# Optimization experiments

Hardware: AMD Instinct MI355X
Metric: run time of the kernel (lower is better)

## Reference

```python
import jax, jax.numpy as jnp
import numpy as np
from jax import lax


def ternarize(w):
    """Standard TWN ternarization with straight-through estimator.
    delta = 0.7*mean(|w|); alpha = mean(|w|) over kept entries; w_t = alpha*sign(w)*mask.
    """
    a = jnp.abs(w)
    delta = 0.7 * a.mean()
    mask = (a > delta).astype(w.dtype)
    alpha = (a * mask).sum() / jnp.maximum(mask.sum(), 1.0)
    wt = alpha * jnp.sign(w) * mask
    return w + lax.stop_gradient(wt - w)  # STE


def conv3x3(x, w, b):
    y = lax.conv_general_dilated(x, ternarize(w), window_strides=(1, 1),
                                 padding=((1, 1), (1, 1)),
                                 dimension_numbers=('NCHW', 'OIHW', 'NCHW'))
    return y + b[None, :, None, None]


def maxpool2(x):
    return lax.reduce_window(x, -jnp.inf, lax.max, (1, 1, 2, 2), (1, 1, 2, 2), 'VALID')


def setup_inputs() -> dict:
    key = jax.random.key(0)
    ks = jax.random.split(key, 11)
    s = lambda k, shape, scale: jax.random.normal(k, shape, dtype=jnp.float32) * scale
    return {
        'x':   s(ks[0], (1024, 3, 32, 32), 1.0),
        'w1':  s(ks[1], (64, 3, 3, 3), 0.1),
        'b1':  s(ks[2], (64,), 0.01),
        'w2':  s(ks[3], (128, 64, 3, 3), 0.05),
        'b2':  s(ks[4], (128,), 0.01),
        'w3':  s(ks[5], (256, 128, 3, 3), 0.03),
        'b3':  s(ks[6], (256,), 0.01),
        'wf1': s(ks[7], (256, 4096), 0.02),
        'bf1': s(ks[8], (256,), 0.01),
        'wf2': s(ks[9], (10, 256), 0.06),
        'bf2': s(ks[10], (10,), 0.01),
    }


def reference(x, w1, b1, w2, b2, w3, b3, wf1, bf1, wf2, bf2):
    x = maxpool2(jax.nn.relu(conv3x3(x, w1, b1)))   # [B,64,16,16]
    x = maxpool2(jax.nn.relu(conv3x3(x, w2, b2)))   # [B,128,8,8]
    x = maxpool2(jax.nn.relu(conv3x3(x, w3, b3)))   # [B,256,4,4]
    x = x.reshape(-1, 256 * 4 * 4)
    x = jax.nn.relu(x @ ternarize(wf1).T + bf1)     # [B,256]
    return x @ ternarize(wf2).T + bf2               # [B,10]
```

## Files before the change

kernel.cpp:

```cpp
#include <hip/hip_runtime.h>
#include <hip/hip_bf16.h>


typedef __attribute__((ext_vector_type(8))) short short8;
typedef __attribute__((ext_vector_type(4))) float f32x4;
typedef __attribute__((ext_vector_type(4))) int i32x4;

#define GLOAD_LDS16(g, l)                                              \
    __builtin_amdgcn_global_load_lds(                                  \
        (const __attribute__((address_space(1))) void*)(g),            \
        (__attribute__((address_space(3))) void*)(l), 16, 0, 0)

__device__ __forceinline__ unsigned short f2bf(float x) {
    unsigned u = __float_as_uint(x);
    return (unsigned short)((u + 0x7fffu + ((u >> 16) & 1u)) >> 16);
}
__device__ __forceinline__ float bf2f(unsigned short b) {
    return __uint_as_float(((unsigned)b) << 16);
}

__device__ __forceinline__ float calc_S1(const double* __restrict__ scr,
                                         float amaxx) {
    const int* ii = (const int*)(scr + 20);
    const double c2 = scr[2];
    const float alpha1 = (float)(scr[1] / (c2 > 1.0 ? c2 : 1.0));
    const float ub = alpha1 * (float)ii[3] * amaxx + __int_as_float(ii[6]);
    return 32512.0f / fmaxf(ub, 1e-30f);
}
__device__ __forceinline__ float calc_S2(const double* __restrict__ scr,
                                         float amax1) {
    const int* ii = (const int*)(scr + 20);
    const double c2 = scr[6];
    const float alpha2 = (float)(scr[5] / (c2 > 1.0 ? c2 : 1.0));
    const float ub = alpha2 * (float)ii[4] * amax1 + __int_as_float(ii[7]);
    return 32512.0f / fmaxf(ub, 1e-30f);
}
__device__ __forceinline__ float calc_S3(const double* __restrict__ scr,
                                         float amax2) {
    const int* ii = (const int*)(scr + 20);
    const double c2 = scr[10];
    const float alpha3 = (float)(scr[9] / (c2 > 1.0 ? c2 : 1.0));
    const float ub = alpha3 * (float)ii[5] * amax2 + __int_as_float(ii[8]);
    return 32512.0f / fmaxf(ub, 1e-30f);
}

#define WS_W1B   0
#define N_W1B    2048
#define WS_W2P   (WS_W1B + N_W1B)
#define N_W2P    (9*128*64)
#define WS_W3P   (WS_W2P + N_W2P)
#define N_W3P    (9*256*128)
#define WS_WTF1  (WS_W3P + N_W3P)
#define N_WTF1   (256*4096)
#define WS_WTF2  (WS_WTF1 + N_WTF1)
#define N_WTF2   (10*256)
#define WS_A1    (WS_WTF2 + N_WTF2)
#define N_A1     (1024*256*64)
#define WS_A2    (WS_A1 + N_A1)
#define N_A2     (1024*64*128)
#define WS_A3    (WS_A2 + N_A2)
#define N_A3     (1024*16*256)
#define WS_F1    (WS_A3 + N_A3)
#define N_F1     (1024*256)
#define WS_SCR   (WS_F1 + N_F1)

#define FC1_S    8

struct TernArgs {
    const float* w[6];
    int n[6];
};

__global__ void tern_stats1(TernArgs ta, double* __restrict__ scr) {
    const int wi = blockIdx.y;
    const float* __restrict__ w = ta.w[wi];
    const int n = ta.n[wi];
    __shared__ double red[4];
    const int lane = threadIdx.x & 63, wv = threadIdx.x >> 6;
    if (wi == 5) {
        float m = 0.f;
        for (int i = blockIdx.x * blockDim.x + threadIdx.x; i < n;
             i += gridDim.x * blockDim.x)
            m = fmaxf(m, fabsf(w[i]));
        #pragma unroll
        for (int off = 32; off > 0; off >>= 1)
            m = fmaxf(m, __shfl_down(m, off, 64));
        if (lane == 0) red[wv] = (double)m;
        __syncthreads();
        if (threadIdx.x == 0) {
            float mm = (float)fmax(fmax(red[0], red[1]), fmax(red[2], red[3]));
            atomicMax((int*)(scr + 20), __float_as_int(mm));
        }
        return;
    }
    double s = 0.0;
    for (int i = blockIdx.x * blockDim.x + threadIdx.x; i < n;
         i += gridDim.x * blockDim.x)
        s += (double)fabsf(w[i]);
    #pragma unroll
    for (int off = 32; off > 0; off >>= 1) s += __shfl_down(s, off, 64);
    if (lane == 0) red[wv] = s;
    __syncthreads();
    if (threadIdx.x == 0)
        atomicAdd(scr + wi * 4, red[0] + red[1] + red[2] + red[3]);
}

__global__ void tern_stats2(TernArgs ta,
                            const float* __restrict__ b1v,
                            const float* __restrict__ b2v,
                            const float* __restrict__ b3v,
                            signed char* __restrict__ w1b,
                            signed char* __restrict__ w2p8,
                            signed char* __restrict__ w3p8,
                            signed char* __restrict__ wtf1b8,
                            signed char* __restrict__ wtf2b8,
                            double* __restrict__ scr) {
    const int wi = blockIdx.y;
    const int lane = threadIdx.x & 63, wv = threadIdx.x >> 6;

    if (wi == 5) {
        int* ii = (int*)(scr + 20);
        const int gw = blockIdx.x * 4 + wv;
        if (gw < 64) {
            const float d = (float)(0.7 * scr[0] / 1728.0);
            const float* row = ta.w[0] + gw * 27;
            int c = (lane < 27) ? (fabsf(row[lane]) > d ? 1 : 0) : 0;
            #pragma unroll
            for (int off = 32; off > 0; off >>= 1)
                c += __shfl_down(c, off, 64);
            if (lane == 0) atomicMax(ii + 3, c);
        } else if (gw < 192) {
            const float d = (float)(0.7 * scr[4] / 73728.0);
            const float* row = ta.w[1] + (long)(gw - 64) * 576;
            int c = 0;
            for (int k = lane; k < 576; k += 64)
                c += (fabsf(row[k]) > d) ? 1 : 0;
            #pragma unroll
            for (int off = 32; off > 0; off >>= 1)
                c += __shfl_down(c, off, 64);
            if (lane == 0) atomicMax(ii + 4, c);
        } else if (gw < 448) {
            const float d = (float)(0.7 * scr[8] / 294912.0);
            const float* row = ta.w[2] + (long)(gw - 192) * 1152;
            int c = 0;
            for (int k = lane; k < 1152; k += 64)
                c += (fabsf(row[k]) > d) ? 1 : 0;
            #pragma unroll
            for (int off = 32; off > 0; off >>= 1)
                c += __shfl_down(c, off, 64);
            if (lane == 0) atomicMax(ii + 5, c);
        } else if (gw < 451) {
            const float* bv = (gw == 448) ? b1v : (gw == 449) ? b2v : b3v;
            const int nb = (gw == 448) ? 64 : (gw == 449) ? 128 : 256;
            float m = 0.f;
            for (int k = lane; k < nb; k += 64) m = fmaxf(m, fabsf(bv[k]));
            #pragma unroll
            for (int off = 32; off > 0; off >>= 1)
                m = fmaxf(m, __shfl_down(m, off, 64));
            if (lane == 0)
                atomicMax(ii + 6 + (gw - 448), __float_as_int(m));
        }
        return;
    }

    const float* __restrict__ w = ta.w[wi];
    const int n = ta.n[wi];
    const float delta = (float)(0.7 * scr[wi * 4] / (double)n);

    if (wi == 0) {
        const int z0 = blockIdx.x * blockDim.x + threadIdx.x;
        const int zstride = gridDim.x * blockDim.x;
        for (int i = z0; i < 8192; i += zstride) {
            const int k = i & 63;
            const int plane = i >> 12;
            const bool sign_slot = plane == 0 ? (k < 27)
                                              : (k >= 32 && k < 59);
            if (!sign_slot) w1b[i] = 0;
        }
    }

    double ms = 0.0, cnt = 0.0;
    for (int i = blockIdx.x * blockDim.x + threadIdx.x; i < n;
         i += gridDim.x * blockDim.x) {
        const float v = w[i];
        const float a = fabsf(v);
        const bool mk = (a > delta);
        if (mk) { ms += (double)a; cnt += 1.0; }
        const signed char s = mk ? (v > 0.0f ? 1 : -1) : 0;
        if (wi == 0) {
            const int co = i / 27;
            const int kp = i % 27;
            w1b[co * 64 + kp] = s;
            w1b[4096 + co * 64 + 32 + kp] = s;
        } else if (wi == 1 || wi == 2) {
            const int CIc = (wi == 1) ? 64 : 128;
            const int COc = (wi == 1) ? 128 : 256;
            signed char* dst = (wi == 1) ? w2p8 : w3p8;
            const int co = i / (CIc * 9);
            const int r = i % (CIc * 9);
            const int ci = r / 9, tap = r % 9;
            dst[(tap * COc + co) * CIc + ci] = s;
        } else if (wi == 3) {
            const int j = i >> 12;
            const int k = i & 4095;
            const int px = k & 15, c = k >> 4;
            wtf1b8[(long)j * 4096 + px * 256 + c] = s;
        } else {
            wtf2b8[i] = s;
        }
    }
    #pragma unroll
    for (int off = 32; off > 0; off >>= 1) {
        ms += __shfl_down(ms, off, 64);
        cnt += __shfl_down(cnt, off, 64);
    }
    __shared__ double redm[4], redc[4];
    if (lane == 0) { redm[wv] = ms; redc[wv] = cnt; }
    __syncthreads();
    if (threadIdx.x == 0) {
        atomicAdd(scr + wi * 4 + 1, redm[0] + redm[1] + redm[2] + redm[3]);
        atomicAdd(scr + wi * 4 + 2, redc[0] + redc[1] + redc[2] + redc[3]);
    }
}

__global__ __launch_bounds__(256) void conv1_i8(
        const float* __restrict__ x,
        const signed char* __restrict__ w1b,
        const float* __restrict__ bias,
        const double* __restrict__ scr,
        const int* __restrict__ amax_x,
        int* __restrict__ amax_out,
        signed char* __restrict__ a1q) {
    constexpr int PL = 3472;
    __shared__ __align__(16) char X[2 * PL];
    __shared__ float redm[4];

    const int b = blockIdx.x;
    const int tid = threadIdx.x;
    const float amx = fmaxf(__int_as_float(*amax_x), 1e-30f);
    const float S = 32512.0f / amx;
    const float S1 = calc_S1(scr, __int_as_float(*amax_x));

    for (int i = tid; i < 2 * PL / 16; i += 256)
        ((int4*)X)[i] = make_int4(0, 0, 0, 0);
    __syncthreads();

    for (int i = tid; i < 768; i += 256) {
        const float4 v = ((const float4*)(x + (long)b * 3072))[i];
        const int e = i * 4;
        const int ci = e >> 10;
        const int rem = e & 1023;
        const int h = rem >> 5, w = rem & 31;
        const int base = ci * 1156 + (h + 1) * 34 + (w + 1);
        const float f[4] = {v.x, v.y, v.z, v.w};
        #pragma unroll
        for (int j = 0; j < 4; j++) {
            const int q = __float2int_rn(f[j] * S);
            const int ql = (q << 24) >> 24;
            const int qh = (q - ql) >> 8;
            X[base + j] = (char)ql;
            X[PL + base + j] = (char)qh;
        }
    }
    __syncthreads();

    const int lane = tid & 63;
    const int wid = tid >> 6;
    const int lm = lane & 15;
    const int kg = lane >> 4;

    const int poff = (kg >= 2) ? PL : 0;
    int cst[16];
    #pragma unroll
    for (int j = 0; j < 16; j++) {
        const int kp = (kg & 1) * 16 + j;
        cst[j] = (kp < 27)
                     ? ((kp / 9) * 1156 + ((kp % 9) / 3) * 34 + (kp % 9) % 3)
                     : 0;
    }

    i32x4 BL[4], BH[4];
    #pragma unroll
    for (int nt = 0; nt < 4; nt++) {
        const int co = nt * 16 + lm;
        BL[nt] = *(const i32x4*)(w1b + (long)co * 64 + kg * 16);
        BH[nt] = *(const i32x4*)(w1b + 4096 + (long)co * 64 + kg * 16);
    }

    const double c2 = scr[2];
    const float alpha = (float)(scr[1] / (c2 > 1.0 ? c2 : 1.0));
    const float dq = alpha / S;
    float tmax = 0.f;
    signed char* yb = a1q + (long)b * 32768;

    for (int tt = 0; tt < 16; ++tt) {
        const int t = wid * 16 + tt;
        const int pp = t * 4 + (lm >> 2);
        const int sub = lm & 3;
        const int h = 2 * (pp >> 4) + (sub >> 1);
        const int w = 2 * (pp & 15) + (sub & 1);
        const int base = poff + h * 34 + w;
        unsigned d[4] = {0u, 0u, 0u, 0u};
        #pragma unroll
        for (int j = 0; j < 16; j++) {
            const unsigned byte = (unsigned char)X[base + cst[j]];
            d[j >> 2] |= byte << ((j & 3) * 8);
        }
        i32x4 Af;
        Af[0] = (int)d[0]; Af[1] = (int)d[1];
        Af[2] = (int)d[2]; Af[3] = (int)d[3];

        const int opp = t * 4 + kg;
        const int ho = opp >> 4, wo = opp & 15;
        signed char* yrow = yb + ((long)ho * 2048) + wo * 64;
        #pragma unroll
        for (int nt = 0; nt < 4; nt++) {
            i32x4 aL = 0, aH = 0;
            aL = __builtin_amdgcn_mfma_i32_16x16x64_i8(Af, BL[nt], aL, 0, 0, 0);
            aH = __builtin_amdgcn_mfma_i32_16x16x64_i8(Af, BH[nt], aH, 0, 0, 0);
            const int s0 = aH[0] * 256 + aL[0];
            const int s1 = aH[1] * 256 + aL[1];
            const int s2 = aH[2] * 256 + aL[2];
            const int s3 = aH[3] * 256 + aL[3];
            int sm = s0 > s1 ? s0 : s1;
            const int sn = s2 > s3 ? s2 : s3;
            sm = sm > sn ? sm : sn;
            const int co = nt * 16 + lm;
            const float o = fmaxf(dq * (float)sm + bias[co], 0.f);
            tmax = fmaxf(tmax, o);
            const int q = (int)(o * S1 + 0.5f);
            const int ql = (q << 24) >> 24;
            const int qh = (q + 128) >> 8;
            const int slot = (nt + ((wo + 1) >> 1) + 2 * (ho + 1)) & 3;
            const int off = slot * 16 + lm;
            yrow[off] = (char)ql;
            yrow[1024 + off] = (char)qh;
        }
    }

    #pragma unroll
    for (int off = 32; off > 0; off >>= 1)
        tmax = fmaxf(tmax, __shfl_down(tmax, off, 64));
    if (lane == 0) redm[wid] = tmax;
    __syncthreads();
    if (tid == 0) {
        float m = fmaxf(fmaxf(redm[0], redm[1]), fmaxf(redm[2], redm[3]));
        atomicMax(amax_out, __float_as_int(m));
    }
}

template <int CI, int HI, int CO, int HB, int WM, int WN, int MODE, int WIDX>
__global__ __launch_bounds__(256, 2) void conv_i8(
        const signed char* __restrict__ xin,
        const signed char* __restrict__ wp,
        const float* __restrict__ bias,
        const double* __restrict__ scr,
        const int* __restrict__ amax_x,
        const int* __restrict__ amax_1,
        int* __restrict__ amax_2,
        void* __restrict__ yout) {
    constexpr int CH8 = CI / 64;
    constexpr int NITER = 9 * CH8;
    constexpr int HR = HI / HB;
    constexpr int ROWS = HR + 2;
    constexpr int COLS = HI + 2;
    constexpr int NPIX = ROWS * COLS;
    constexpr int PSTR = NPIX * 64 + 32;
    constexpr int PO = HI / 2;
    constexpr int POR = HR / 2;
    constexpr int MT = 4, NT = 4;
    constexpr int NPL = 2 * CH8;
    constexpr int RWQ = HI * 64 * 2;
    static_assert(WM * WN == 4, "4 waves");
    static_assert(WM * 64 == HR * HI, "M covers slab pixels");
    static_assert(WN * 64 == CO, "N covers all co");
    static_assert(MODE != 0 || (CI == 64 && RWQ == 2048), "conv2 shape");
    static_assert(MODE != 1 || (CI == 128 && HB == 1), "conv3 shape");
    static_assert(HB <= 2, "row compaction assumes <=1 invalid row per end");
    static_assert((COLS & 1) == 0, "swizzle parity uses even COLS");

    __shared__ __align__(16) char X[NPL * PSTR];
    __shared__ __align__(16) char RAW2[(MODE == 1) ? 16384 : 16];
    __shared__ float redm[4];

    const int bimg = blockIdx.x / HB;
    const int hb = blockIdx.x % HB;
    const int tid = threadIdx.x;
    const int lane = tid & 63;
    const int wid = tid >> 6;

    const float S_in = (MODE == 0)
                           ? calc_S1(scr, __int_as_float(*amax_x))
                           : calc_S2(scr, __int_as_float(*amax_1));

    const int rlo = (hb == 0) ? 1 : 0;
    const int rhi = (hb == HB - 1) ? (ROWS - 1) : ROWS;

    if (MODE == 0) {
        for (int r = rlo; r < rhi; r++) {
            #pragma unroll
            for (int pl = 0; pl < 2; pl++) {
                if (wid == ((r * 2 + pl) & 3)) {
                    const int h = hb * HR + r - 1;
                    const signed char* src = xin +
                        (long)(bimg * HI + h) * RWQ + pl * 1024 + lane * 16;
                    GLOAD_LDS16(src, &X[pl * PSTR + (r * COLS + 1) * 64]);
                }
            }
        }
    } else {
        #pragma unroll
        for (int j = 0; j < 16; j++) {
            if (wid == (j & 3)) {
                const signed char* src = xin + (long)bimg * 16384 +
                                         j * 1024 + lane * 16;
                GLOAD_LDS16(src, &RAW2[j * 1024]);
            }
        }
    }

    {
        const int nfull = ((hb == 0) ? 1 : 0) + ((hb == HB - 1) ? 1 : 0);
        const int NP1 = ROWS * 2;
        const int NPZ = NP1 + nfull * (COLS - 2);
        for (int i = tid; i < NPZ * NPL * 4; i += 256) {
            const int u = i & 3;
            const int t = i >> 2;
            const int g = t % NPL;
            const int e = t / NPL;
            int p;
            if (e < NP1) {
                const int row = e >> 1;
                p = row * COLS + ((e & 1) ? (COLS - 1) : 0);
            } else {
                const int e2 = e - NP1;
                const int inFirst = (hb == 0) && (e2 < COLS - 2);
                const int fr = inFirst ? 0 : (ROWS - 1);
                const int cc = inFirst ? e2
                                       : (e2 - ((hb == 0) ? (COLS - 2) : 0));
                p = fr * COLS + 1 + cc;
            }
            *(int4*)&X[g * PSTR + p * 64 + u * 16] = make_int4(0, 0, 0, 0);
        }
    }

    if (MODE == 1) {
        __syncthreads();
        #pragma unroll
        for (int k = 0; k < 16; k++) {
            const int v = tid + k * 256;
            const int h = v >> 9;
            const int r = v & 511;
            const int g = r >> 7;
            const int b4 = (r & 127) << 2;
            const unsigned d = *(const unsigned*)&RAW2[v << 2];
            *(unsigned*)&X[g * PSTR + ((h + 1) * COLS + 1) * 64 + b4] = d;
        }
    }
    __syncthreads();

    const int wm = (WM == 1) ? 0 : (wid >> 1);
    const int wn = (WM == 1) ? wid : (wid & 1);
    const int lm = lane & 15;
    const int kg = lane >> 4;

    int pq[MT];
    #pragma unroll
    for (int mt = 0; mt < MT; mt++) {
        const int m = (wm * MT + mt) * 16 + lm;
        const int pp = m >> 2, sub = m & 3;
        const int lph = pp / PO, lpw = pp % PO;
        const int h = 2 * lph + (sub >> 1);
        const int w = 2 * lpw + (sub & 1);
        pq[mt] = ((h * COLS + w) << 6) | ((h & 1) << 3) | (w & 7);
    }
    const signed char* bp[NT];
    #pragma unroll
    for (int nt = 0; nt < NT; nt++) {
        const int co = (wn * NT + nt) * 16 + lm;
        bp[nt] = wp + (long)co * CI + kg * 16;
    }

    i32x4 accL[MT][NT], accH[MT][NT];
    #pragma unroll
    for (int mt = 0; mt < MT; mt++)
        #pragma unroll
        for (int nt = 0; nt < NT; nt++) { accL[mt][nt] = 0; accH[mt][nt] = 0; }

    i32x4 Bb[2][NT];
    #pragma unroll
    for (int nt = 0; nt < NT; nt++) Bb[0][nt] = *(const i32x4*)(bp[nt]);

    #pragma unroll 2
    for (int it = 0; it < NITER; ++it) {
        const int cur = it & 1, nxt = cur ^ 1;
        if (it + 1 < NITER) {
            const int it1 = it + 1;
            const int tap = it1 / CH8, ch1 = it1 % CH8;
            const int woff = tap * CO * CI + ch1 * 64;
            #pragma unroll
            for (int nt = 0; nt < NT; nt++)
                Bb[nxt][nt] = *(const i32x4*)(bp[nt] + woff);
        }
        const int tap = it / CH8, ch = it % CH8;
        const int ty = tap / 3, tx = tap % 3;
        const int DT = (ty * COLS + tx) << 6;
        const int typ = ty & 1;
        int ao[MT];
        #pragma unroll
        for (int mt = 0; mt < MT; mt++) {
            const int q = pq[mt];
            const int slot = (kg + ((((q >> 3) & 1) + typ) & 1) * 2 +
                              (((q & 7) + tx) >> 1)) & 3;
            ao[mt] = (q & ~63) + DT + (slot << 4);
        }
        {
            i32x4 Af[MT];
            #pragma unroll
            for (int mt = 0; mt < MT; mt++)
                Af[mt] = *(const i32x4*)&X[ch * PSTR + ao[mt]];
            #pragma unroll
            for (int mt = 0; mt < MT; mt++)
                #pragma unroll
                for (int nt = 0; nt < NT; nt++)
                    accL[mt][nt] = __builtin_amdgcn_mfma_i32_16x16x64_i8(
                        Af[mt], Bb[cur][nt], accL[mt][nt], 0, 0, 0);
        }
        {
            i32x4 Af[MT];
            #pragma unroll
            for (int mt = 0; mt < MT; mt++)
                Af[mt] = *(const i32x4*)&X[(CH8 + ch) * PSTR + ao[mt]];
            #pragma unroll
            for (int mt = 0; mt < MT; mt++)
                #pragma unroll
                for (int nt = 0; nt < NT; nt++)
                    accH[mt][nt] = __builtin_amdgcn_mfma_i32_16x16x64_i8(
                        Af[mt], Bb[cur][nt], accH[mt][nt], 0, 0, 0);
        }
    }

    const double* wst = scr + WIDX * 4;
    const double c2 = wst[2];
    const float alpha = (float)(wst[1] / (c2 > 1.0 ? c2 : 1.0));
    const float dq = alpha / S_in;
    if (MODE == 0) {
        const float S2 = calc_S2(scr, __int_as_float(*amax_1));
        signed char* oq = (signed char*)yout;
        float tmax = 0.f;
        #pragma unroll
        for (int mt = 0; mt < MT; mt++) {
            const int pp = (wm * MT + mt) * 4 + kg;
            const int lph = pp / PO, lpw = pp % PO;
            const int h = hb * POR + lph;
            const int w = lpw;
            #pragma unroll
            for (int nt = 0; nt < NT; nt++) {
                const int co2 = (wn * NT + nt) * 16 + lm;
                const i32x4 aL = accL[mt][nt], aH = accH[mt][nt];
                int s0 = aH[0] * 256 + aL[0];
                int s1 = aH[1] * 256 + aL[1];
                int s2 = aH[2] * 256 + aL[2];
                int s3 = aH[3] * 256 + aL[3];
                int sm = s0 > s1 ? s0 : s1;
                int sn = s2 > s3 ? s2 : s3;
                sm = sm > sn ? sm : sn;
                const float o = fmaxf(dq * (float)sm + bias[co2], 0.f);
                tmax = fmaxf(tmax, o);
                const int q = (int)(o * S2 + 0.5f);
                const int ql = (q << 24) >> 24;
                const int qh = (q + 128) >> 8;
                const int slot = (((co2 >> 4) & 3) + ((w + 1) >> 1) +
                                  2 * (h + 1)) & 3;
                const long base = (long)bimg * 16384 + h * 2048 +
                                  (co2 >> 6) * 512 + w * 64 + slot * 16 +
                                  (co2 & 15);
                oq[base] = (char)ql;
                oq[base + 1024] = (char)qh;
            }
        }
        #pragma unroll
        for (int off = 32; off > 0; off >>= 1)
            tmax = fmaxf(tmax, __shfl_down(tmax, off, 64));
        if (lane == 0) redm[wid] = tmax;
        __syncthreads();
        if (tid == 0) {
            float m = fmaxf(fmaxf(redm[0], redm[1]), fmaxf(redm[2], redm[3]));
            atomicMax(amax_2, __float_as_int(m));
        }
    } else {
        const float S3 = calc_S3(scr, __int_as_float(*amax_2));
        signed char* oq = (signed char*)yout;
        #pragma unroll
        for (int mt = 0; mt < MT; mt++) {
            const int pp = (wm * MT + mt) * 4 + kg;
            const int lph = pp / PO, lpw = pp % PO;
            const int gpp = (hb * POR + lph) * PO + lpw;
            signed char* yr = oq + (long)bimg * 8192 + gpp * 512;
            #pragma unroll
            for (int nt = 0; nt < NT; nt++) {
                const int co = (wn * NT + nt) * 16 + lm;
                const i32x4 aL = accL[mt][nt], aH = accH[mt][nt];
                int s0 = aH[0] * 256 + aL[0];
                int s1 = aH[1] * 256 + aL[1];
                int s2 = aH[2] * 256 + aL[2];
                int s3 = aH[3] * 256 + aL[3];
                int sm = s0 > s1 ? s0 : s1;
                int sn = s2 > s3 ? s2 : s3;
                sm = sm > sn ? sm : sn;
                const float o = fmaxf(dq * (float)sm + bias[co], 0.f);
                const int q = (int)(o * S3 + 0.5f);
                const int ql = (q << 24) >> 24;
                const int qh = (q + 128) >> 8;
                yr[co] = (char)ql;
                yr[256 + co] = (char)qh;
            }
        }
    }
}

template <int S>
__global__ __launch_bounds__(256) void fc1_i8(
        const signed char* __restrict__ A,
        const signed char* __restrict__ Bw,
        float* __restrict__ parts) {
    constexpr int KCH = 4096 / S;
    constexpr int NCH = KCH / 64;
    const int m0 = blockIdx.x * 64;
    const int n0 = blockIdx.y * 64;
    const int s = blockIdx.z;
    const int tid = threadIdx.x;
    const int lane = tid & 63, wid = tid >> 6;
    const int wm = wid >> 1, wn = wid & 1;
    const int lm = lane & 15, kg = lane >> 4;

    const int k0 = s * KCH;
    const signed char* ap[2];
    const signed char* bp[2];
    #pragma unroll
    for (int t = 0; t < 2; t++) {
        ap[t] = A + (long)(m0 + wm * 32 + t * 16 + lm) * 8192;
        bp[t] = Bw + (long)(n0 + wn * 32 + t * 16 + lm) * 4096 + k0 + kg * 16;
    }

    i32x4 accL[2][2], accH[2][2];
    #pragma unroll
    for (int mt = 0; mt < 2; mt++)
        #pragma unroll
        for (int nt = 0; nt < 2; nt++) { accL[mt][nt] = 0; accH[mt][nt] = 0; }

    #pragma unroll
    for (int ch = 0; ch < NCH; ++ch) {
        const int kb = k0 + ch * 64;
        const int aoff = (kb >> 8) * 512 + (kb & 255) + kg * 16;
        i32x4 Ah[2], Al[2], Bb[2];
        #pragma unroll
        for (int t = 0; t < 2; t++) {
            Al[t] = *(const i32x4*)(ap[t] + aoff);
            Ah[t] = *(const i32x4*)(ap[t] + aoff + 256);
            Bb[t] = *(const i32x4*)(bp[t] + ch * 64);
        }
        #pragma unroll
        for (int mt = 0; mt < 2; mt++)
            #pragma unroll
            for (int nt = 0; nt < 2; nt++) {
                accH[mt][nt] = __builtin_amdgcn_mfma_i32_16x16x64_i8(
                    Ah[mt], Bb[nt], accH[mt][nt], 0, 0, 0);
                accL[mt][nt] = __builtin_amdgcn_mfma_i32_16x16x64_i8(
                    Al[mt], Bb[nt], accL[mt][nt], 0, 0, 0);
            }
    }

    #pragma unroll
    for (int mt = 0; mt < 2; mt++) {
        #pragma unroll
        for (int r = 0; r < 4; r++) {
            const int b = m0 + wm * 32 + mt * 16 + kg * 4 + r;
            #pragma unroll
            for (int nt = 0; nt < 2; nt++) {
                const int j = n0 + wn * 32 + nt * 16 + lm;
                const int sum = accH[mt][nt][r] * 256 + accL[mt][nt][r];
                parts[((long)s * 1024 + b) * 256 + j] = (float)sum;
            }
        }
    }
}

template <int S>
__global__ __launch_bounds__(256) void fc2_fused(
        const float* __restrict__ parts,
        const double* __restrict__ scr,
        const int* __restrict__ amax_2,
        const float* __restrict__ bf1v,
        const signed char* __restrict__ wtf2b8,
        const float* __restrict__ bf2v,
        float* __restrict__ out) {
    __shared__ float sf[256];
    const int b = blockIdx.x;
    const int j = threadIdx.x;
    float s = 0.f;
    #pragma unroll
    for (int p = 0; p < S; p++)
        s += parts[(long)p * 262144 + (long)b * 256 + j];
    const double c2 = scr[14];
    const float alpha = (float)(scr[13] / (c2 > 1.0 ? c2 : 1.0));
    const float S3 = calc_S3(scr, __int_as_float(*amax_2));
    sf[j] = fmaxf(alpha * s / S3 + bf1v[j], 0.f);
    __syncthreads();
    const double c4 = scr[18];
    const float alpha4 = (float)(scr[17] / (c4 > 1.0 ? c4 : 1.0));
    const int lane = threadIdx.x & 63, wid = threadIdx.x >> 6;
    for (int k = wid; k < 10; k += 4) {
        const signed char* wr = wtf2b8 + k * 256;
        float acc = 0.f;
        #pragma unroll
        for (int t = 0; t < 4; t++)
            acc += sf[lane + t * 64] * (float)wr[lane + t * 64];
        #pragma unroll
        for (int off = 32; off > 0; off >>= 1)
            acc += __shfl_down(acc, off, 64);
        if (lane == 0) out[(long)b * 10 + k] = acc * alpha4 + bf2v[k];
    }
}

extern "C" void kernel_launch(void* const* d_in, const int* in_sizes, int n_in,
                              void* d_out, int out_size, void* d_ws, size_t ws_size,
                              hipStream_t stream) {
    const float* x   = (const float*)d_in[0];
    const float* w1  = (const float*)d_in[1];
    const float* b1  = (const float*)d_in[2];
    const float* w2  = (const float*)d_in[3];
    const float* b2  = (const float*)d_in[4];
    const float* w3  = (const float*)d_in[5];
    const float* b3  = (const float*)d_in[6];
    const float* wf1 = (const float*)d_in[7];
    const float* bf1 = (const float*)d_in[8];
    const float* wf2 = (const float*)d_in[9];
    const float* bf2 = (const float*)d_in[10];
    float* out = (float*)d_out;
    float* ws = (float*)d_ws;

    const int B = 1024;

    signed char*    w1b    = (signed char*)(ws + WS_W1B);
    signed char*    w2p8   = (signed char*)(ws + WS_W2P);
    signed char*    w3p8   = (signed char*)(ws + WS_W3P);
    signed char*    wtf1b8 = (signed char*)(ws + WS_WTF1);
    signed char*    wtf2b8 = (signed char*)(ws + WS_WTF2);
    signed char*    a1q    = (signed char*)(ws + WS_A1);
    signed char*    a2q    = (signed char*)(ws + WS_A2);
    signed char*    a3q    = (signed char*)(ws + WS_A3);
    double*         scr    = (double*)(ws + WS_SCR);
    int*            iscr   = (int*)(scr + 20);
    int*            amaxx  = iscr;
    int*            amax1  = iscr + 1;
    int*            amax2  = iscr + 2;
    float*          parts  = ws + WS_A1;

    hipMemsetAsync(scr, 0, 26 * sizeof(double), stream);

    TernArgs ta;
    ta.w[0] = w1;  ta.n[0] = 64 * 27;
    ta.w[1] = w2;  ta.n[1] = 128 * 64 * 9;
    ta.w[2] = w3;  ta.n[2] = 256 * 128 * 9;
    ta.w[3] = wf1; ta.n[3] = 256 * 4096;
    ta.w[4] = wf2; ta.n[4] = 10 * 256;
    ta.w[5] = x;   ta.n[5] = 1024 * 3 * 32 * 32;

    hipLaunchKernelGGL(tern_stats1, dim3(128, 6), dim3(256), 0, stream, ta, scr);
    hipLaunchKernelGGL(tern_stats2, dim3(128, 6), dim3(256), 0, stream,
                       ta, b1, b2, b3, w1b, w2p8, w3p8, wtf1b8, wtf2b8, scr);

    hipLaunchKernelGGL(conv1_i8, dim3(B), dim3(256), 0, stream,
                       x, w1b, b1, scr, amaxx, amax1, a1q);

    hipLaunchKernelGGL((conv_i8<64, 16, 128, 2, 2, 2, 0, 1>), dim3(B * 2),
                       dim3(256), 0, stream, a1q, w2p8, b2, scr, amaxx,
                       amax1, amax2, a2q);

    hipLaunchKernelGGL((conv_i8<128, 8, 256, 1, 1, 4, 1, 2>), dim3(B),
                       dim3(256), 0, stream, a2q, w3p8, b3, scr, amaxx,
                       amax1, amax2, a3q);

    hipLaunchKernelGGL((fc1_i8<FC1_S>), dim3(16, 4, FC1_S), dim3(256), 0, stream,
                       a3q, wtf1b8, parts);

    hipLaunchKernelGGL((fc2_fused<FC1_S>), dim3(B), dim3(256), 0, stream,
                       parts, scr, amax2, bf1, wtf2b8, bf2, out);
}
```

Before: 261.1 us.

## Fuse fc1 and fc2 into one kernel, dropping split-K partials

```diff
diff --git a/kernel.cpp b/kernel.cpp
--- a/kernel.cpp
+++ b/kernel.cpp
@@ -63,8 +63,6 @@
 #define WS_F1    (WS_A3 + N_A3)
 #define N_F1     (1024*256)
 #define WS_SCR   (WS_F1 + N_F1)
-
-#define FC1_S    8
 
 struct TernArgs {
     const float* w[6];
@@ -619,107 +617,77 @@
     }
 }
 
-template <int S>
-__global__ __launch_bounds__(256) void fc1_i8(
+__global__ __launch_bounds__(512) void fc1fc2_i8(
         const signed char* __restrict__ A,
         const signed char* __restrict__ Bw,
-        float* __restrict__ parts) {
-    constexpr int KCH = 4096 / S;
-    constexpr int NCH = KCH / 64;
-    const int m0 = blockIdx.x * 64;
-    const int n0 = blockIdx.y * 64;
-    const int s = blockIdx.z;
-    const int tid = threadIdx.x;
-    const int lane = tid & 63, wid = tid >> 6;
-    const int wm = wid >> 1, wn = wid & 1;
-    const int lm = lane & 15, kg = lane >> 4;
-
-    const int k0 = s * KCH;
-    const signed char* ap[2];
-    const signed char* bp[2];
-    #pragma unroll
-    for (int t = 0; t < 2; t++) {
-        ap[t] = A + (long)(m0 + wm * 32 + t * 16 + lm) * 8192;
-        bp[t] = Bw + (long)(n0 + wn * 32 + t * 16 + lm) * 4096 + k0 + kg * 16;
-    }
-
-    i32x4 accL[2][2], accH[2][2];
-    #pragma unroll
-    for (int mt = 0; mt < 2; mt++)
-        #pragma unroll
-        for (int nt = 0; nt < 2; nt++) { accL[mt][nt] = 0; accH[mt][nt] = 0; }
-
-    #pragma unroll
-    for (int ch = 0; ch < NCH; ++ch) {
-        const int kb = k0 + ch * 64;
-        const int aoff = (kb >> 8) * 512 + (kb & 255) + kg * 16;
-        i32x4 Ah[2], Al[2], Bb[2];
-        #pragma unroll
-        for (int t = 0; t < 2; t++) {
-            Al[t] = *(const i32x4*)(ap[t] + aoff);
-            Ah[t] = *(const i32x4*)(ap[t] + aoff + 256);
-            Bb[t] = *(const i32x4*)(bp[t] + ch * 64);
-        }
-        #pragma unroll
-        for (int mt = 0; mt < 2; mt++)
-            #pragma unroll
-            for (int nt = 0; nt < 2; nt++) {
-                accH[mt][nt] = __builtin_amdgcn_mfma_i32_16x16x64_i8(
-                    Ah[mt], Bb[nt], accH[mt][nt], 0, 0, 0);
-                accL[mt][nt] = __builtin_amdgcn_mfma_i32_16x16x64_i8(
-                    Al[mt], Bb[nt], accL[mt][nt], 0, 0, 0);
-            }
-    }
-
-    #pragma unroll
-    for (int mt = 0; mt < 2; mt++) {
-        #pragma unroll
-        for (int r = 0; r < 4; r++) {
-            const int b = m0 + wm * 32 + mt * 16 + kg * 4 + r;
-            #pragma unroll
-            for (int nt = 0; nt < 2; nt++) {
-                const int j = n0 + wn * 32 + nt * 16 + lm;
-                const int sum = accH[mt][nt][r] * 256 + accL[mt][nt][r];
-                parts[((long)s * 1024 + b) * 256 + j] = (float)sum;
-            }
-        }
-    }
-}
-
-template <int S>
-__global__ __launch_bounds__(256) void fc2_fused(
-        const float* __restrict__ parts,
         const double* __restrict__ scr,
         const int* __restrict__ amax_2,
         const float* __restrict__ bf1v,
         const signed char* __restrict__ wtf2b8,
         const float* __restrict__ bf2v,
         float* __restrict__ out) {
-    __shared__ float sf[256];
-    const int b = blockIdx.x;
-    const int j = threadIdx.x;
-    float s = 0.f;
-    #pragma unroll
-    for (int p = 0; p < S; p++)
-        s += parts[(long)p * 262144 + (long)b * 256 + j];
+    __shared__ float hbuf[16][257];
+
+    const int m0 = blockIdx.x * 16;
+    const int tid = threadIdx.x;
+    const int lane = tid & 63, wn = tid >> 6;
+    const int lm = lane & 15, kg = lane >> 4;
+
+    const signed char* ap = A + (long)(m0 + lm) * 8192;
+    const signed char* bp[2];
+    #pragma unroll
+    for (int nt = 0; nt < 2; nt++)
+        bp[nt] = Bw + (long)(wn * 32 + nt * 16 + lm) * 4096 + kg * 16;
+
+    i32x4 accL[2], accH[2];
+    #pragma unroll
+    for (int nt = 0; nt < 2; nt++) { accL[nt] = 0; accH[nt] = 0; }
+
+    #pragma unroll 4
+    for (int ch = 0; ch < 64; ++ch) {
+        const int aoff = (ch >> 2) * 512 + ((ch & 3) << 6) + kg * 16;
+        const i32x4 Al = *(const i32x4*)(ap + aoff);
+        const i32x4 Ah = *(const i32x4*)(ap + aoff + 256);
+        i32x4 Bb[2];
+        #pragma unroll
+        for (int nt = 0; nt < 2; nt++)
+            Bb[nt] = *(const i32x4*)(bp[nt] + ch * 64);
+        #pragma unroll
+        for (int nt = 0; nt < 2; nt++) {
+            accL[nt] = __builtin_amdgcn_mfma_i32_16x16x64_i8(
+                Al, Bb[nt], accL[nt], 0, 0, 0);
+            accH[nt] = __builtin_amdgcn_mfma_i32_16x16x64_i8(
+                Ah, Bb[nt], accH[nt], 0, 0, 0);
+        }
+    }
+
     const double c2 = scr[14];
     const float alpha = (float)(scr[13] / (c2 > 1.0 ? c2 : 1.0));
     const float S3 = calc_S3(scr, __int_as_float(*amax_2));
-    sf[j] = fmaxf(alpha * s / S3 + bf1v[j], 0.f);
+    #pragma unroll
+    for (int nt = 0; nt < 2; nt++) {
+        const int ch = wn * 32 + nt * 16 + lm;
+        const float bj = bf1v[ch];
+        #pragma unroll
+        for (int r = 0; r < 4; r++) {
+            const int img = kg * 4 + r;
+            const int sum = accH[nt][r] * 256 + accL[nt][r];
+            hbuf[img][ch] = fmaxf(alpha * (float)sum / S3 + bj, 0.f);
+        }
+    }
     __syncthreads();
-    const double c4 = scr[18];
-    const float alpha4 = (float)(scr[17] / (c4 > 1.0 ? c4 : 1.0));
-    const int lane = threadIdx.x & 63, wid = threadIdx.x >> 6;
-    for (int k = wid; k < 10; k += 4) {
+
+    if (tid < 160) {
+        const int img = tid / 10;
+        const int k = tid % 10;
+        const double c4 = scr[18];
+        const float alpha4 = (float)(scr[17] / (c4 > 1.0 ? c4 : 1.0));
         const signed char* wr = wtf2b8 + k * 256;
         float acc = 0.f;
-        #pragma unroll
-        for (int t = 0; t < 4; t++)
-            acc += sf[lane + t * 64] * (float)wr[lane + t * 64];
-        #pragma unroll
-        for (int off = 32; off > 0; off >>= 1)
-            acc += __shfl_down(acc, off, 64);
-        if (lane == 0) out[(long)b * 10 + k] = acc * alpha4 + bf2v[k];
+        #pragma unroll 8
+        for (int c = 0; c < 256; c++)
+            acc += hbuf[img][c] * (float)wr[c];
+        out[(long)(m0 + img) * 10 + k] = acc * alpha4 + bf2v[k];
     }
 }
 
@@ -755,7 +723,6 @@
     int*            amaxx  = iscr;
     int*            amax1  = iscr + 1;
     int*            amax2  = iscr + 2;
-    float*          parts  = ws + WS_A1;
 
     hipMemsetAsync(scr, 0, 26 * sizeof(double), stream);
 
@@ -782,9 +749,6 @@
                        dim3(256), 0, stream, a2q, w3p8, b3, scr, amaxx,
                        amax1, amax2, a3q);
 
-    hipLaunchKernelGGL((fc1_i8<FC1_S>), dim3(16, 4, FC1_S), dim3(256), 0, stream,
-                       a3q, wtf1b8, parts);
-
-    hipLaunchKernelGGL((fc2_fused<FC1_S>), dim3(B), dim3(256), 0, stream,
-                       parts, scr, amax2, bf1, wtf2b8, bf2, out);
-}
+    hipLaunchKernelGGL(fc1fc2_i8, dim3(64), dim3(512), 0, stream,
+                       a3q, wtf1b8, scr, amax2, bf1, wtf2b8, bf2, out);
+}
```

After: 304.5 us. 16.6% more time.
